# Performance work log

Hardware: AMD Instinct MI355X
Metric: run time of the kernel (lower is better)

The kernel has to match this reference:

```python
import jax, jax.numpy as jnp
import numpy as np

LN_EPS = 1e-5

def _ln(x, g, b):
    m = x.mean(-1, keepdims=True)
    v = x.var(-1, keepdims=True)
    return (x - m) * jax.lax.rsqrt(v + LN_EPS) * g + b

def _sru_layer(x, W, vc, bias, g, be):
    # x: (L, B, d); W: (d, k*h) with k=3 (d==h) or k=4 (d!=h)
    L, B, _ = x.shape
    h = vc.shape[0] // 2
    xn = _ln(x, g, be)
    k = W.shape[1] // h
    U = (xn @ W).reshape(L, B, k, h)
    u0, u1, u2 = U[:, :, 0], U[:, :, 1], U[:, :, 2]
    res = U[:, :, 3] if k == 4 else xn
    vf, vr = vc[:h], vc[h:]
    bf, br = bias[:h], bias[h:]
    def step(c, inp):
        a0, a1, a2, rt = inp
        f = jax.nn.sigmoid(a1 + vf * c + bf)
        r = jax.nn.sigmoid(a2 + vr * c + br)
        c2 = f * c + (1.0 - f) * a0
        return c2, r * c2 + (1.0 - r) * rt
    _, hs = jax.lax.scan(step, jnp.zeros((B, h), x.dtype), (u0, u1, u2, res))
    return hs  # (L, B, h)

def _lstm(x, Wih, Whh, bih, bhh):
    # x: (L, B, d); PyTorch gate order i, f, g, o
    L, B, _ = x.shape
    H = Whh.shape[1]
    pre = x @ Wih.T + (bih + bhh)  # (L, B, 4H)
    def step(carry, p):
        hp, cp = carry
        gates = p + hp @ Whh.T
        i, f, g, o = jnp.split(gates, 4, axis=-1)
        c = jax.nn.sigmoid(f) * cp + jax.nn.sigmoid(i) * jnp.tanh(g)
        hn = jax.nn.sigmoid(o) * jnp.tanh(c)
        return (hn, c), hn
    z = jnp.zeros((B, H), x.dtype)
    _, hs = jax.lax.scan(step, (z, z), pre)
    return hs

def setup_inputs() -> dict:
    key = jax.random.key(0)
    ks = jax.random.split(key, 12)
    B, T, F, H, LS, V = 16, 1024, 128, 1024, 1024, 1000
    s = 0.05
    inp = {}
    inp['x'] = jax.random.normal(ks[0], (B, T, F), dtype=jnp.float32)
    # first SRU layer (input F != H -> k=4)
    inp['w0'] = jax.random.normal(ks[1], (F, 4 * H), dtype=jnp.float32) * s
    inp['vc0'] = jax.random.normal(ks[2], (2 * H,), dtype=jnp.float32) * s
    inp['b0'] = jnp.zeros((2 * H,), jnp.float32)
    inp['g0'] = jnp.ones((F,), jnp.float32)
    inp['be0'] = jnp.zeros((F,), jnp.float32)
    # 6 stacked SRU layers with d==h (3 remaining first_layer + 3 sru_layers)
    inp['Ws'] = jax.random.normal(ks[3], (6, H, 3 * H), dtype=jnp.float32) * s
    inp['VCs'] = jax.random.normal(ks[4], (6, 2 * H), dtype=jnp.float32) * s
    inp['Bs'] = jnp.zeros((6, 2 * H), jnp.float32)
    inp['Gs'] = jnp.ones((6, H), jnp.float32)
    inp['Bes'] = jnp.zeros((6, H), jnp.float32)
    # LSTM
    inp['Wih'] = jax.random.normal(ks[5], (4 * LS, H), dtype=jnp.float32) * s
    inp['Whh'] = jax.random.normal(ks[6], (4 * LS, LS), dtype=jnp.float32) * s
    inp['bih'] = jnp.zeros((4 * LS,), jnp.float32)
    inp['bhh'] = jnp.zeros((4 * LS,), jnp.float32)
    # classifier: LayerNorm + Linear(no bias) to V+1
    inp['gh'] = jnp.ones((LS,), jnp.float32)
    inp['bh'] = jnp.zeros((LS,), jnp.float32)
    inp['Wout'] = jax.random.normal(ks[7], (LS, V + 1), dtype=jnp.float32) * s
    return inp

def reference(x, w0, vc0, b0, g0, be0, Ws, VCs, Bs, Gs, Bes,
              Wih, Whh, bih, bhh, gh, bh, Wout):
    t = jnp.transpose(x, (1, 0, 2))  # (T, B, F)
    t = _sru_layer(t, w0, vc0, b0, g0, be0)
    for i in range(3):
        t = _sru_layer(t, Ws[i], VCs[i], Bs[i], Gs[i], Bes[i])
    # AvgPool1d(kernel=2, stride=2) over time
    L = t.shape[0]
    t = t[: (L // 2) * 2].reshape(L // 2, 2, t.shape[1], t.shape[2]).mean(axis=1)
    for i in range(3, 6):
        t = _sru_layer(t, Ws[i], VCs[i], Bs[i], Gs[i], Bes[i])
    t = _lstm(t, Wih, Whh, bih, bhh)
    t = jnp.transpose(t, (1, 0, 2))  # (B, T/2, lstm_dim)
    return _ln(t, gh, bh) @ Wout  # (B, T/2, n_vocab+1)
```

## Files before the change

kernel.cpp:

```cpp
#include <hip/hip_runtime.h>

typedef __bf16 bf16x8 __attribute__((ext_vector_type(8)));
typedef float f32x4 __attribute__((ext_vector_type(4)));

__device__ __forceinline__ unsigned short f2bf(float f) {
  unsigned u = __builtin_bit_cast(unsigned, f);
  u += 0x7fffu + ((u >> 16) & 1u);
  return (unsigned short)(u >> 16);
}
__device__ __forceinline__ float bf2f(unsigned short h) {
  unsigned u = ((unsigned)h) << 16;
  return __builtin_bit_cast(float, u);
}
__device__ __forceinline__ float sigmoidf_(float x) {
  return 1.f / (1.f + __expf(-x));
}
__device__ __forceinline__ float tanhf_(float x) {
  return 1.f - 2.f / (__expf(2.f * x) + 1.f);
}


__global__ __launch_bounds__(256) void k_castf(const float* __restrict__ src,
                                               unsigned short* __restrict__ dst, int n4) {
  int i = blockIdx.x * 256 + threadIdx.x;
  if (i < n4) {
    float4 v = ((const float4*)src)[i];
    ushort4 o;
    o.x = f2bf(v.x); o.y = f2bf(v.y); o.z = f2bf(v.z); o.w = f2bf(v.w);
    ((ushort4*)dst)[i] = o;
  }
}

__global__ void k_cast_t(const float* __restrict__ src, unsigned short* __restrict__ dst,
                         int K, int N) {
  __shared__ float tile[32][33];
  int nx = blockIdx.x * 32, ky = blockIdx.y * 32;
  int tx = threadIdx.x, ty = threadIdx.y;
  #pragma unroll
  for (int j = 0; j < 32; j += 8) {
    int n = nx + tx, k = ky + ty + j;
    tile[ty + j][tx] = (n < N) ? src[(long)k * N + n] : 0.f;
  }
  __syncthreads();
  #pragma unroll
  for (int j = 0; j < 32; j += 8) {
    int n = nx + ty + j, k = ky + tx;
    dst[(long)n * K + k] = f2bf(tile[tx][ty + j]);
  }
}


__global__ __launch_bounds__(128) void k_ln0(const float* __restrict__ x,
                                             unsigned short* __restrict__ out,
                                             const float* __restrict__ g,
                                             const float* __restrict__ be) {
  int row = blockIdx.x;
  int t = row >> 4, b = row & 15;
  const float* src = x + ((long)b * 1024 + t) * 128;
  int i = threadIdx.x;
  float v = src[i];
  float s = v, q = v * v;
  #pragma unroll
  for (int off = 32; off > 0; off >>= 1) {
    s += __shfl_down(s, off);
    q += __shfl_down(q, off);
  }
  __shared__ float red[4];
  int wv = i >> 6;
  if ((i & 63) == 0) { red[wv] = s; red[2 + wv] = q; }
  __syncthreads();
  float S = red[0] + red[1], Q = red[2] + red[3];
  float mean = S * (1.f / 128.f);
  float var = Q * (1.f / 128.f) - mean * mean;
  float rs = rsqrtf(var + 1e-5f);
  out[(long)row * 128 + i] = f2bf((v - mean) * rs * g[i] + be[i]);
}

__global__ __launch_bounds__(256) void k_ln(const float* __restrict__ in,
                                            unsigned short* __restrict__ out16,
                                            const float* __restrict__ g,
                                            const float* __restrict__ be, int avg) {
  int row = blockIdx.x;
  int tid = threadIdx.x;
  int col = tid * 4;
  float xv[4];
  if (avg) {
    int l = row >> 4, b = row & 15;
    const float* r0 = in + ((long)(2 * l) * 16 + b) * 1024;
    const float* r1 = r0 + 16 * 1024;
    float4 a = *(const float4*)(r0 + col);
    float4 bb = *(const float4*)(r1 + col);
    xv[0] = 0.5f * (a.x + bb.x);
    xv[1] = 0.5f * (a.y + bb.y);
    xv[2] = 0.5f * (a.z + bb.z);
    xv[3] = 0.5f * (a.w + bb.w);
  } else {
    float4 a = *(const float4*)(in + (long)row * 1024 + col);
    xv[0] = a.x; xv[1] = a.y; xv[2] = a.z; xv[3] = a.w;
  }
  float s = xv[0] + xv[1] + xv[2] + xv[3];
  float q = xv[0]*xv[0] + xv[1]*xv[1] + xv[2]*xv[2] + xv[3]*xv[3];
  #pragma unroll
  for (int off = 32; off > 0; off >>= 1) {
    s += __shfl_down(s, off);
    q += __shfl_down(q, off);
  }
  __shared__ float red[8];
  int wv = tid >> 6;
  if ((tid & 63) == 0) { red[wv] = s; red[4 + wv] = q; }
  __syncthreads();
  float S = red[0] + red[1] + red[2] + red[3];
  float Q = red[4] + red[5] + red[6] + red[7];
  float mean = S * (1.f / 1024.f);
  float var = Q * (1.f / 1024.f) - mean * mean;
  float rs = rsqrtf(var + 1e-5f);
  ushort4 o;
  o.x = f2bf((xv[0] - mean) * rs * g[col + 0] + be[col + 0]);
  o.y = f2bf((xv[1] - mean) * rs * g[col + 1] + be[col + 1]);
  o.z = f2bf((xv[2] - mean) * rs * g[col + 2] + be[col + 2]);
  o.w = f2bf((xv[3] - mean) * rs * g[col + 3] + be[col + 3]);
  *(ushort4*)(out16 + (long)row * 1024 + col) = o;
}

template <int MODE>
__global__ __launch_bounds__(256) void k_gemm(const unsigned short* __restrict__ A,
                                              const unsigned short* __restrict__ Bt,
                                              void* __restrict__ Cout,
                                              const float* __restrict__ bias1,
                                              const float* __restrict__ bias2,
                                              int M, int N, int K) {
  __shared__ unsigned short As[64][72];
  __shared__ unsigned short Bs[64][72];
  const int bn = blockIdx.x * 64, bm = blockIdx.y * 64;
  const int tid = threadIdx.x;
  const int wave = tid >> 6, lane = tid & 63;
  const int wm = (wave >> 1) * 32, wn = (wave & 1) * 32;
  const int l15 = lane & 15, kq = lane >> 4;
  f32x4 zz = {0.f, 0.f, 0.f, 0.f};
  f32x4 acc00 = zz, acc01 = zz, acc10 = zz, acc11 = zz;
  const int r0 = tid >> 3, c0 = (tid & 7) * 8;
  for (int kb = 0; kb < K; kb += 64) {
    *(uint4*)&As[r0][c0]      = *(const uint4*)&A[(long)(bm + r0) * K + kb + c0];
    *(uint4*)&As[r0 + 32][c0] = *(const uint4*)&A[(long)(bm + r0 + 32) * K + kb + c0];
    *(uint4*)&Bs[r0][c0]      = *(const uint4*)&Bt[(long)(bn + r0) * K + kb + c0];
    *(uint4*)&Bs[r0 + 32][c0] = *(const uint4*)&Bt[(long)(bn + r0 + 32) * K + kb + c0];
    __syncthreads();
    #pragma unroll
    for (int kk = 0; kk < 2; kk++) {
      const int kcol = kk * 32 + kq * 8;
      bf16x8 a0 = *(const bf16x8*)&As[wm + l15][kcol];
      bf16x8 a1 = *(const bf16x8*)&As[wm + 16 + l15][kcol];
      bf16x8 b0 = *(const bf16x8*)&Bs[wn + l15][kcol];
      bf16x8 b1 = *(const bf16x8*)&Bs[wn + 16 + l15][kcol];
      acc00 = __builtin_amdgcn_mfma_f32_16x16x32_bf16(a0, b0, acc00, 0, 0, 0);
      acc01 = __builtin_amdgcn_mfma_f32_16x16x32_bf16(a0, b1, acc01, 0, 0, 0);
      acc10 = __builtin_amdgcn_mfma_f32_16x16x32_bf16(a1, b0, acc10, 0, 0, 0);
      acc11 = __builtin_amdgcn_mfma_f32_16x16x32_bf16(a1, b1, acc11, 0, 0, 0);
    }
    __syncthreads();
  }
  f32x4 accs[2][2] = {{acc00, acc01}, {acc10, acc11}};
  #pragma unroll
  for (int mt = 0; mt < 2; mt++)
    #pragma unroll
    for (int nt = 0; nt < 2; nt++) {
      #pragma unroll
      for (int r = 0; r < 4; r++) {
        int gm = bm + wm + mt * 16 + kq * 4 + r;
        int gn = bn + wn + nt * 16 + l15;
        float v = accs[mt][nt][r];
        if (MODE == 0) {
          ((float*)Cout)[(long)gm * N + gn] = v;
        } else if (MODE == 1) {
          v += bias1[gn] + bias2[gn];
          ((float*)Cout)[(long)gm * N + gn] = v;
        } else {
          if (gn < 1001) {
            long oi = ((long)(gm & 15) * 512 + (gm >> 4)) * 1001 + gn;
            ((float*)Cout)[oi] = v;
          }
        }
      }
    }
}

__global__ __launch_bounds__(64) void k_scan(const float* __restrict__ U,
                                             const unsigned short* __restrict__ Res16,
                                             const float* __restrict__ vc,
                                             const float* __restrict__ bias,
                                             float* __restrict__ Hout,
                                             unsigned short* __restrict__ H16,
                                             float* __restrict__ cbuf,
                                             int Lc, int k4, int first) {
  int tid = blockIdx.x * 64 + threadIdx.x;
  int b = tid >> 10, hc = tid & 1023;
  float vf = vc[hc], vr = vc[1024 + hc];
  float bfv = bias[hc], brv = bias[1024 + hc];
  const int k = k4 ? 4 : 3;
  const long strideT = 16L * k * 1024;
  const long base0 = (long)b * k * 1024 + hc;
  const long rbase = (long)b * 1024 + hc;
  const long rstride = 16 * 1024;
  float c = first ? 0.f : cbuf[tid];
  for (int t0 = 0; t0 < Lc; t0 += 8) {
    float u0[8], u1[8], u2[8], rr[8];
    #pragma unroll
    for (int j = 0; j < 8; j++) {
      long o = base0 + (long)(t0 + j) * strideT;
      u0[j] = U[o];
      u1[j] = U[o + 1024];
      u2[j] = U[o + 2048];
      rr[j] = k4 ? U[o + 3072] : bf2f(Res16[rbase + (long)(t0 + j) * rstride]);
    }
    #pragma unroll
    for (int j = 0; j < 8; j++) {
      float f = sigmoidf_(u1[j] + vf * c + bfv);
      float r = sigmoidf_(u2[j] + vr * c + brv);
      c = f * c + (1.f - f) * u0[j];
      float h = r * c + (1.f - r) * rr[j];
      long oo = rbase + (long)(t0 + j) * rstride;
      Hout[oo] = h;
      if (H16) H16[oo] = f2bf(h);
    }
  }
  cbuf[tid] = c;
}

__global__ __launch_bounds__(256) void k_lstm_step(
    const unsigned short* __restrict__ Whhb,
    const float* __restrict__ Prep,
    const unsigned short* __restrict__ hin,
    unsigned short* __restrict__ hout,
    float* __restrict__ cst,
    float* __restrict__ HsOutp) {
  const int tid = threadIdx.x;
  const int wave = tid >> 6, lane = tid & 63;
  const int j = blockIdx.x;
  const int c0 = j * 4;
  const int l15 = lane & 15, kq = lane >> 4;
  const int wrow = (l15 >> 2) * 1024 + c0 + (l15 & 3);
  f32x4 acc = {0.f, 0.f, 0.f, 0.f};
  const unsigned short* hp = hin + l15 * 1024 + wave * 256 + kq * 8;
  const unsigned short* wp = Whhb + (long)wrow * 1024 + wave * 256 + kq * 8;
  #pragma unroll
  for (int kb = 0; kb < 256; kb += 32) {
    bf16x8 a = *(const bf16x8*)(hp + kb);
    bf16x8 w = *(const bf16x8*)(wp + kb);
    acc = __builtin_amdgcn_mfma_f32_16x16x32_bf16(a, w, acc, 0, 0, 0);
  }
  __shared__ float P[4][16][16];
  __shared__ float G[16][16];
  #pragma unroll
  for (int r = 0; r < 4; r++) {
    int m = kq * 4 + r;
    P[wave][m][l15] = acc[r];
  }
  __syncthreads();
  {
    int m = tid >> 4, col = tid & 15;
    int gate = col >> 2, ch = c0 + (col & 3);
    float pre = Prep[(long)m * 4096 + gate * 1024 + ch];
    G[m][col] = P[0][m][col] + P[1][m][col] + P[2][m][col] + P[3][m][col] + pre;
  }
  __syncthreads();
  if (tid < 64) {
    int m = tid & 15, chl = tid >> 4;
    float ig = G[m][0 * 4 + chl];
    float fg = G[m][1 * 4 + chl];
    float gg = G[m][2 * 4 + chl];
    float og = G[m][3 * 4 + chl];
    long ci = (long)m * 1024 + c0 + chl;
    float cold = cst[ci];
    float cn = sigmoidf_(fg) * cold + sigmoidf_(ig) * tanhf_(gg);
    float hn = sigmoidf_(og) * tanhf_(cn);
    cst[ci] = cn;
    hout[ci] = f2bf(hn);
    HsOutp[(long)m * 1024 + c0 + chl] = hn;
  }
}


extern "C" void kernel_launch(void* const* d_in, const int* in_sizes, int n_in,
                              void* d_out, int out_size, void* d_ws, size_t ws_size,
                              hipStream_t stream) {
  const float* x    = (const float*)d_in[0];
  const float* w0   = (const float*)d_in[1];
  const float* vc0  = (const float*)d_in[2];
  const float* b0   = (const float*)d_in[3];
  const float* g0   = (const float*)d_in[4];
  const float* be0  = (const float*)d_in[5];
  const float* Ws   = (const float*)d_in[6];
  const float* VCs  = (const float*)d_in[7];
  const float* Bsi  = (const float*)d_in[8];
  const float* Gs   = (const float*)d_in[9];
  const float* Bes  = (const float*)d_in[10];
  const float* Wih  = (const float*)d_in[11];
  const float* Whh  = (const float*)d_in[12];
  const float* bih  = (const float*)d_in[13];
  const float* bhh  = (const float*)d_in[14];
  const float* gh   = (const float*)d_in[15];
  const float* bh   = (const float*)d_in[16];
  const float* Wout = (const float*)d_in[17];

  char* ws = (char*)d_ws;
  size_t off = 0;
  auto alloc = [&](size_t bytes) {
    size_t r = off;
    off += (bytes + 255) & ~(size_t)255;
    return r;
  };
  unsigned short* W0t   = (unsigned short*)(ws + alloc(4096UL * 128 * 2));
  unsigned short* Wst   = (unsigned short*)(ws + alloc(6UL * 3072 * 1024 * 2));
  unsigned short* Wihb  = (unsigned short*)(ws + alloc(4096UL * 1024 * 2));
  unsigned short* Whhb  = (unsigned short*)(ws + alloc(4096UL * 1024 * 2));
  unsigned short* Woutt = (unsigned short*)(ws + alloc(1024UL * 1024 * 2));
  unsigned short* Xn    = (unsigned short*)(ws + alloc(16384UL * 1024 * 2));
  float*          Hbuf  = (float*)(ws + alloc(16384UL * 1024 * 4));
  float*          Ubuf  = (float*)(ws + alloc(4096UL * 4096 * 4));
  unsigned short* hb0   = (unsigned short*)(ws + alloc(16UL * 1024 * 2));
  unsigned short* hb1   = (unsigned short*)(ws + alloc(16UL * 1024 * 2));
  float*          cst   = (float*)(ws + alloc(16UL * 1024 * 4));
  float*          cscan = (float*)(ws + alloc(16UL * 1024 * 4));
  float*          HsOut = Hbuf;
  unsigned short* H16l6 = Xn + 8192L * 1024;
  unsigned short* LNout = Xn;

  k_cast_t<<<dim3(4096 / 32, 128 / 32), dim3(32, 8), 0, stream>>>(w0, W0t, 128, 4096);
  for (int i = 0; i < 6; i++)
    k_cast_t<<<dim3(3072 / 32, 1024 / 32), dim3(32, 8), 0, stream>>>(
        Ws + (long)i * 1024 * 3072, Wst + (long)i * 3072 * 1024, 1024, 3072);
  k_cast_t<<<dim3(1024 / 32, 1024 / 32), dim3(32, 8), 0, stream>>>(Wout, Woutt, 1024, 1001);
  k_castf<<<4096, 256, 0, stream>>>(Wih, Wihb, 4096 * 1024 / 4);
  k_castf<<<4096, 256, 0, stream>>>(Whh, Whhb, 4096 * 1024 / 4);
  hipMemsetAsync(hb0, 0, 32768 + 32768 + 65536, stream);

  const int CH_T = 256;
  const int CH_R = CH_T * 16;

  k_ln0<<<16384, 128, 0, stream>>>(x, Xn, g0, be0);
  for (int c = 0; c < 4; c++) {
    k_gemm<0><<<dim3(4096 / 64, CH_R / 64), 256, 0, stream>>>(
        Xn + (long)c * CH_R * 128, W0t, Ubuf, nullptr, nullptr, CH_R, 4096, 128);
    k_scan<<<256, 64, 0, stream>>>(Ubuf, nullptr, vc0, b0,
                                   Hbuf + (long)c * CH_R * 1024, nullptr, cscan,
                                   CH_T, 1, c == 0);
  }

  for (int i = 0; i < 6; i++) {
    int L = (i < 3) ? 1024 : 512;
    int rows = L * 16;
    int avg = (i == 3) ? 1 : 0;
    k_ln<<<rows, 256, 0, stream>>>(Hbuf, Xn, Gs + i * 1024, Bes + i * 1024, avg);
    int nch = rows / CH_R;
    for (int c = 0; c < nch; c++) {
      k_gemm<0><<<dim3(3072 / 64, CH_R / 64), 256, 0, stream>>>(
          Xn + (long)c * CH_R * 1024, Wst + (long)i * 3072 * 1024, Ubuf, nullptr, nullptr,
          CH_R, 3072, 1024);
      k_scan<<<256, 64, 0, stream>>>(Ubuf, Xn + (long)c * CH_R * 1024,
                                     VCs + i * 2048, Bsi + i * 2048,
                                     Hbuf + (long)c * CH_R * 1024,
                                     (i == 5) ? (H16l6 + (long)c * CH_R * 1024) : nullptr,
                                     cscan, CH_T, 0, c == 0);
    }
  }

  const int LCH_T = 128, LCH_R = LCH_T * 16;
  for (int c = 0; c < 4; c++) {
    k_gemm<1><<<dim3(4096 / 64, LCH_R / 64), 256, 0, stream>>>(
        H16l6 + (long)c * LCH_R * 1024, Wihb, Ubuf, bih, bhh, LCH_R, 4096, 1024);
    for (int tl = 0; tl < LCH_T; tl++) {
      int tg = c * LCH_T + tl;
      unsigned short* hin = (tg & 1) ? hb1 : hb0;
      unsigned short* hout = (tg & 1) ? hb0 : hb1;
      k_lstm_step<<<256, 256, 0, stream>>>(Whhb, Ubuf + (long)tl * 16 * 4096, hin, hout,
                                           cst, HsOut + (long)tg * 16 * 1024);
    }
  }

  k_ln<<<8192, 256, 0, stream>>>(HsOut, LNout, gh, bh, 0);
  k_gemm<2><<<dim3(1024 / 64, 8192 / 64), 256, 0, stream>>>(LNout, Woutt, d_out, nullptr,
                                                            nullptr, 8192, 1024, 1024);
}
```

Before: 6.449 ms.

## Enlarge GEMM tiles to 128x128 and load tiles directly into LDS

The bf16 MFMA GEMM block tile grows from 64x64 to 128x128. Each wave now computes a 64x64 sub-tile with a 4x4 grid of 16x16x32 MFMAs, which raises operand reuse and cuts global traffic per flop. Tile loads now use global_load_lds 16-byte direct-to-LDS transfers instead of going through registers. The LDS row padding is dropped so each wave's writes stay contiguous, which may cause bank conflicts on the fragment reads. The larger accumulator set raises register pressure, and all GEMM launch grids are resized to match.

Result: faster. 6.257 ms (-3.0%).

```diff
diff --git a/kernel.cpp b/kernel.cpp
--- a/kernel.cpp
+++ b/kernel.cpp
@@ -17,6 +17,10 @@
 }
 __device__ __forceinline__ float tanhf_(float x) {
   return 1.f - 2.f / (__expf(2.f * x) + 1.f);
+}
+__device__ __forceinline__ void gload16(const unsigned short* g, unsigned short* l) {
+  __builtin_amdgcn_global_load_lds((const __attribute__((address_space(1))) void*)g,
+                                   (__attribute__((address_space(3))) void*)l, 16, 0, 0);
 }
 
 
@@ -129,46 +133,50 @@
                                               const float* __restrict__ bias1,
                                               const float* __restrict__ bias2,
                                               int M, int N, int K) {
-  __shared__ unsigned short As[64][72];
-  __shared__ unsigned short Bs[64][72];
-  const int bn = blockIdx.x * 64, bm = blockIdx.y * 64;
+  __shared__ unsigned short As[128][64];
+  __shared__ unsigned short Bs[128][64];
+  const int bn = blockIdx.x * 128, bm = blockIdx.y * 128;
   const int tid = threadIdx.x;
   const int wave = tid >> 6, lane = tid & 63;
-  const int wm = (wave >> 1) * 32, wn = (wave & 1) * 32;
+  const int wm = (wave >> 1) * 64, wn = (wave & 1) * 64;
   const int l15 = lane & 15, kq = lane >> 4;
-  f32x4 zz = {0.f, 0.f, 0.f, 0.f};
-  f32x4 acc00 = zz, acc01 = zz, acc10 = zz, acc11 = zz;
-  const int r0 = tid >> 3, c0 = (tid & 7) * 8;
+  f32x4 acc[4][4] = {};
+  const int r0 = tid >> 3;
+  const int c0 = (tid & 7) * 8;
+  const unsigned short* Ap = A + (long)(bm + r0) * K + c0;
+  const unsigned short* Bp = Bt + (long)(bn + r0) * K + c0;
   for (int kb = 0; kb < K; kb += 64) {
-    *(uint4*)&As[r0][c0]      = *(const uint4*)&A[(long)(bm + r0) * K + kb + c0];
-    *(uint4*)&As[r0 + 32][c0] = *(const uint4*)&A[(long)(bm + r0 + 32) * K + kb + c0];
-    *(uint4*)&Bs[r0][c0]      = *(const uint4*)&Bt[(long)(bn + r0) * K + kb + c0];
-    *(uint4*)&Bs[r0 + 32][c0] = *(const uint4*)&Bt[(long)(bn + r0 + 32) * K + kb + c0];
+    #pragma unroll
+    for (int i = 0; i < 4; i++) {
+      gload16(Ap + (long)(i * 32) * K + kb, &As[i * 32 + r0][c0]);
+      gload16(Bp + (long)(i * 32) * K + kb, &Bs[i * 32 + r0][c0]);
+    }
     __syncthreads();
     #pragma unroll
     for (int kk = 0; kk < 2; kk++) {
       const int kcol = kk * 32 + kq * 8;
-      bf16x8 a0 = *(const bf16x8*)&As[wm + l15][kcol];
-      bf16x8 a1 = *(const bf16x8*)&As[wm + 16 + l15][kcol];
-      bf16x8 b0 = *(const bf16x8*)&Bs[wn + l15][kcol];
-      bf16x8 b1 = *(const bf16x8*)&Bs[wn + 16 + l15][kcol];
-      acc00 = __builtin_amdgcn_mfma_f32_16x16x32_bf16(a0, b0, acc00, 0, 0, 0);
-      acc01 = __builtin_amdgcn_mfma_f32_16x16x32_bf16(a0, b1, acc01, 0, 0, 0);
-      acc10 = __builtin_amdgcn_mfma_f32_16x16x32_bf16(a1, b0, acc10, 0, 0, 0);
-      acc11 = __builtin_amdgcn_mfma_f32_16x16x32_bf16(a1, b1, acc11, 0, 0, 0);
+      bf16x8 a[4], b[4];
+      #pragma unroll
+      for (int m = 0; m < 4; m++) a[m] = *(const bf16x8*)&As[wm + m * 16 + l15][kcol];
+      #pragma unroll
+      for (int n = 0; n < 4; n++) b[n] = *(const bf16x8*)&Bs[wn + n * 16 + l15][kcol];
+      #pragma unroll
+      for (int m = 0; m < 4; m++)
+        #pragma unroll
+        for (int n = 0; n < 4; n++)
+          acc[m][n] = __builtin_amdgcn_mfma_f32_16x16x32_bf16(a[m], b[n], acc[m][n], 0, 0, 0);
     }
     __syncthreads();
   }
-  f32x4 accs[2][2] = {{acc00, acc01}, {acc10, acc11}};
-  #pragma unroll
-  for (int mt = 0; mt < 2; mt++)
-    #pragma unroll
-    for (int nt = 0; nt < 2; nt++) {
+  #pragma unroll
+  for (int m = 0; m < 4; m++)
+    #pragma unroll
+    for (int n = 0; n < 4; n++) {
       #pragma unroll
       for (int r = 0; r < 4; r++) {
-        int gm = bm + wm + mt * 16 + kq * 4 + r;
-        int gn = bn + wn + nt * 16 + l15;
-        float v = accs[mt][nt][r];
+        int gm = bm + wm + m * 16 + kq * 4 + r;
+        int gn = bn + wn + n * 16 + l15;
+        float v = acc[m][n][r];
         if (MODE == 0) {
           ((float*)Cout)[(long)gm * N + gn] = v;
         } else if (MODE == 1) {
@@ -339,7 +347,7 @@
 
   k_ln0<<<16384, 128, 0, stream>>>(x, Xn, g0, be0);
   for (int c = 0; c < 4; c++) {
-    k_gemm<0><<<dim3(4096 / 64, CH_R / 64), 256, 0, stream>>>(
+    k_gemm<0><<<dim3(4096 / 128, CH_R / 128), 256, 0, stream>>>(
         Xn + (long)c * CH_R * 128, W0t, Ubuf, nullptr, nullptr, CH_R, 4096, 128);
     k_scan<<<256, 64, 0, stream>>>(Ubuf, nullptr, vc0, b0,
                                    Hbuf + (long)c * CH_R * 1024, nullptr, cscan,
@@ -353,7 +361,7 @@
     k_ln<<<rows, 256, 0, stream>>>(Hbuf, Xn, Gs + i * 1024, Bes + i * 1024, avg);
     int nch = rows / CH_R;
     for (int c = 0; c < nch; c++) {
-      k_gemm<0><<<dim3(3072 / 64, CH_R / 64), 256, 0, stream>>>(
+      k_gemm<0><<<dim3(3072 / 128, CH_R / 128), 256, 0, stream>>>(
           Xn + (long)c * CH_R * 1024, Wst + (long)i * 3072 * 1024, Ubuf, nullptr, nullptr,
           CH_R, 3072, 1024);
       k_scan<<<256, 64, 0, stream>>>(Ubuf, Xn + (long)c * CH_R * 1024,
@@ -366,7 +374,7 @@
 
   const int LCH_T = 128, LCH_R = LCH_T * 16;
   for (int c = 0; c < 4; c++) {
-    k_gemm<1><<<dim3(4096 / 64, LCH_R / 64), 256, 0, stream>>>(
+    k_gemm<1><<<dim3(4096 / 128, LCH_R / 128), 256, 0, stream>>>(
         H16l6 + (long)c * LCH_R * 1024, Wihb, Ubuf, bih, bhh, LCH_R, 4096, 1024);
     for (int tl = 0; tl < LCH_T; tl++) {
       int tg = c * LCH_T + tl;
@@ -378,6 +386,6 @@
   }
 
   k_ln<<<8192, 256, 0, stream>>>(HsOut, LNout, gh, bh, 0);
-  k_gemm<2><<<dim3(1024 / 64, 8192 / 64), 256, 0, stream>>>(LNout, Woutt, d_out, nullptr,
-                                                            nullptr, 8192, 1024, 1024);
-}
+  k_gemm<2><<<dim3(1024 / 128, 8192 / 128), 256, 0, stream>>>(LNout, Woutt, d_out, nullptr,
+                                                              nullptr, 8192, 1024, 1024);
+}
```
